# Kernel optimization log

Hardware: AMD Instinct MI355X
Metric: run time of the kernel (lower is better)

The kernel has to match this reference:

```python
import jax, jax.numpy as jnp
import numpy as np

K = 7
KK = K * K  # 49 taps
MID = (KK - 1) // 2  # 24

def _ring_ids():
    # Map each of the 49 kernel taps to its attention ring channel:
    # 0 = center, 1 = inner 3x3 ring, 2 = 5x5 ring, 3 = outer 7x7 ring.
    line7 = [j for j in range(KK) if 0 <= j <= 7 or 13 <= j <= 14 or 20 <= j <= 21 or 27 <= j <= 28 or 34 <= j <= 35 or 41 <= j <= 48]
    line5 = [j for j in range(KK) if 8 <= j <= 12 or j in (15, 19, 22, 26, 29, 33) or 36 <= j <= 40]
    line3 = [j for j in range(KK) if 16 <= j <= 18 or j in (23, 25) or 30 <= j <= 32]
    ring = np.zeros(KK, dtype=np.int32)
    ring[line7] = 3
    ring[line5] = 2
    ring[line3] = 1
    ring[MID] = 0
    return jnp.asarray(ring)

_RING = _ring_ids()


def setup_inputs() -> dict:
    key = jax.random.key(0)
    k1, k2, k3, k4 = jax.random.split(key, 4)
    bs, h, w, iters = 4, 256, 320, 6
    hw = h * w
    return {
        "kernel": jax.random.normal(k1, (bs, KK, hw), dtype=jnp.float32),
        "input": jax.random.normal(k2, (bs, 1, h, w), dtype=jnp.float32),
        "input0": jax.random.normal(k3, (bs, 1, h, w), dtype=jnp.float32),
        "attention": jax.random.uniform(k4, (bs, iters, 4, hw), dtype=jnp.float32),
        "i": 2,
    }


def reference(kernel, input, input0, attention, i):
    bs, _, h, w = input.shape
    hw = h * w
    # im2col: 7x7 patches, stride 1, pad 3 -> [bs, 49, h, w] (C=1 so tap order matches F.unfold)
    patches = jax.lax.conv_general_dilated_patches(
        input, (K, K), (1, 1), [(3, 3), (3, 3)]
    ).reshape(bs, KK, hw)
    # Ring-wise attention scaling of the affinity kernel
    att = attention[:, i]              # [bs, 4, hw]
    scale = att[:, _RING, :]           # [bs, 49, hw]
    new_kernel = kernel * scale
    # Abs-sum normalization over the 49 taps
    new_kernel = new_kernel / jnp.sum(jnp.abs(new_kernel), axis=1, keepdims=True)
    # Replace the center tap with input0 values
    patches = patches.at[:, MID, :].set(input0.reshape(bs, hw))
    # Weighted local sum
    out = jnp.sum(patches * new_kernel, axis=1)
    return out.reshape(bs, 1, h, w)
```

## Files before the change

### kernel.cpp

```cpp
#include <hip/hip_runtime.h>

#define KS   7
#define KK   49
#define MIDJ 24
#define H    256
#define W    320
#define HW   (H * W)
#define BS   4
#define ITERS 6

__global__ __launch_bounds__(256) void dyspn_kernel(
    const float* __restrict__ kern,
    const float* __restrict__ input,
    const float* __restrict__ input0,
    const float* __restrict__ att,
    const int*   __restrict__ i_ptr,
    float*       __restrict__ out)
{
    const int i_sel = *i_ptr;

    int t   = blockIdx.x * blockDim.x + threadIdx.x;
    int idx = t * 2;
    if (idx >= BS * HW) return;

    int b = idx / HW;
    int p = idx - b * HW;
    int y = p / W;
    int x = p - y * W;

    const float* attb = att + ((size_t)(b * ITERS + i_sel)) * 4 * HW + p;
    float2 a0 = *(const float2*)(attb);
    float2 a1 = *(const float2*)(attb + HW);
    float2 a2 = *(const float2*)(attb + 2 * HW);
    float2 a3 = *(const float2*)(attb + 3 * HW);
    const float ar0[4] = {a0.x, a1.x, a2.x, a3.x};
    const float ar1[4] = {a0.y, a1.y, a2.y, a3.y};

    const float* kb  = kern + (size_t)b * KK * HW + p;
    const float* inb = input + (size_t)b * HW;

    float acc0 = 0.f, acc1 = 0.f, den0 = 0.f, den1 = 0.f;

#pragma unroll
    for (int j = 0; j < KK; ++j) {
        const int dy = j / KS - 3;
        const int dx = j % KS - 3;
        const int r  = max(dy < 0 ? -dy : dy,
                           dx < 0 ? -dx : dx);

        float2 kv = *(const float2*)(kb + (size_t)j * HW);
        float v0 = kv.x * ar0[r];
        float v1 = kv.y * ar1[r];
        den0 += fabsf(v0);
        den1 += fabsf(v1);

        float p0, p1;
        if (j == MIDJ) {
            float2 z = *(const float2*)(input0 + (size_t)b * HW + p);
            p0 = z.x; p1 = z.y;
        } else {
            const int yy = y + dy;
            if (yy >= 0 && yy < H) {
                const int x0 = x + dx;
                const int x1 = x0 + 1;
                const float* row = inb + yy * W;
                p0 = (x0 >= 0 && x0 < W) ? row[x0] : 0.f;
                p1 = (x1 >= 0 && x1 < W) ? row[x1] : 0.f;
            } else {
                p0 = 0.f; p1 = 0.f;
            }
        }
        acc0 += v0 * p0;
        acc1 += v1 * p1;
    }

    float2 o;
    o.x = acc0 / den0;
    o.y = acc1 / den1;
    *(float2*)(out + (size_t)b * HW + p) = o;
}

extern "C" void kernel_launch(void* const* d_in, const int* in_sizes, int n_in,
                              void* d_out, int out_size, void* d_ws, size_t ws_size,
                              hipStream_t stream) {
    const float* kern   = (const float*)d_in[0];
    const float* input  = (const float*)d_in[1];
    const float* input0 = (const float*)d_in[2];
    const float* att    = (const float*)d_in[3];
    const int*   i_ptr  = (const int*)d_in[4];
    float* out = (float*)d_out;

    const int total_threads = BS * HW / 2;
    const int block = 256;
    const int grid  = (total_threads + block - 1) / block;

    dyspn_kernel<<<grid, block, 0, stream>>>(kern, input, input0, att, i_ptr, out);
}
```

Measured before the change: 21.54 us.

## Pre-pad input into workspace to remove bounds checks, one pixel per thread

Adds a separate kernel that writes a zero-padded copy of the input into the workspace, so the main kernel can read the 7x7 neighbourhood without bounds checks. The main kernel also moves from two pixels per thread with float2 loads to one pixel per thread with scalar loads. This is meant to cut branch and predicate overhead, at the cost of an extra kernel launch, another pass over the input, and narrower loads. A bounds-checked fallback runs when the workspace is too small.

Measured after the change: 22.43 us. +4.1%, slower.

```diff
diff --git a/kernel.cpp b/kernel.cpp
--- a/kernel.cpp
+++ b/kernel.cpp
@@ -9,7 +9,79 @@
 #define BS   4
 #define ITERS 6
 
+#define PH   (H + 6)
+#define PW   328
+#define XOFF 4
+#define PAD_ELEMS (BS * PH * PW)
+
+__global__ __launch_bounds__(256) void pad_kernel(
+    const float* __restrict__ input,
+    float*       __restrict__ pad)
+{
+    int idx = blockIdx.x * blockDim.x + threadIdx.x;
+    if (idx >= PAD_ELEMS) return;
+    int b  = idx / (PH * PW);
+    int r  = idx - b * (PH * PW);
+    int yp = r / PW;
+    int xp = r - yp * PW;
+    int y  = yp - 3;
+    int x  = xp - XOFF;
+    float v = 0.f;
+    if (y >= 0 && y < H && x >= 0 && x < W)
+        v = input[(size_t)b * HW + y * W + x];
+    pad[idx] = v;
+}
+
 __global__ __launch_bounds__(256) void dyspn_kernel(
+    const float* __restrict__ kern,
+    const float* __restrict__ pad,
+    const float* __restrict__ input0,
+    const float* __restrict__ att,
+    const int*   __restrict__ i_ptr,
+    float*       __restrict__ out)
+{
+    const int i_sel = *i_ptr;
+
+    int idx = blockIdx.x * blockDim.x + threadIdx.x;
+    if (idx >= BS * HW) return;
+
+    int b = idx / HW;
+    int p = idx - b * HW;
+    int y = p / W;
+    int x = p - y * W;
+
+    const float* attb = att + ((size_t)(b * ITERS + i_sel)) * 4 * HW + p;
+    float ar[4];
+    ar[0] = attb[0];
+    ar[1] = attb[HW];
+    ar[2] = attb[2 * HW];
+    ar[3] = attb[3 * HW];
+
+    const float* kb   = kern + (size_t)b * KK * HW + p;
+    const float* padb = pad + (size_t)b * PH * PW + (y + 3) * PW + (x + XOFF);
+    const float  mid  = input0[(size_t)b * HW + p];
+
+    float acc = 0.f, den = 0.f;
+
+#pragma unroll
+    for (int j = 0; j < KK; ++j) {
+        const int dy = j / KS - 3;
+        const int dx = j % KS - 3;
+        const int r  = max(dy < 0 ? -dy : dy,
+                           dx < 0 ? -dx : dx);
+
+        float kv = kb[(size_t)j * HW];
+        float v  = kv * ar[r];
+        den += fabsf(v);
+
+        float pv = (j == MIDJ) ? mid : padb[dy * PW + dx];
+        acc = fmaf(v, pv, acc);
+    }
+
+    out[(size_t)b * HW + p] = acc / den;
+}
+
+__global__ __launch_bounds__(256) void dyspn_kernel_checked(
     const float* __restrict__ kern,
     const float* __restrict__ input,
     const float* __restrict__ input0,
@@ -18,66 +90,37 @@
     float*       __restrict__ out)
 {
     const int i_sel = *i_ptr;
-
-    int t   = blockIdx.x * blockDim.x + threadIdx.x;
-    int idx = t * 2;
+    int idx = blockIdx.x * blockDim.x + threadIdx.x;
     if (idx >= BS * HW) return;
-
     int b = idx / HW;
     int p = idx - b * HW;
     int y = p / W;
     int x = p - y * W;
 
     const float* attb = att + ((size_t)(b * ITERS + i_sel)) * 4 * HW + p;
-    float2 a0 = *(const float2*)(attb);
-    float2 a1 = *(const float2*)(attb + HW);
-    float2 a2 = *(const float2*)(attb + 2 * HW);
-    float2 a3 = *(const float2*)(attb + 3 * HW);
-    const float ar0[4] = {a0.x, a1.x, a2.x, a3.x};
-    const float ar1[4] = {a0.y, a1.y, a2.y, a3.y};
-
+    float ar[4] = {attb[0], attb[HW], attb[2 * HW], attb[3 * HW]};
     const float* kb  = kern + (size_t)b * KK * HW + p;
     const float* inb = input + (size_t)b * HW;
+    const float  mid = input0[(size_t)b * HW + p];
 
-    float acc0 = 0.f, acc1 = 0.f, den0 = 0.f, den1 = 0.f;
-
+    float acc = 0.f, den = 0.f;
 #pragma unroll
     for (int j = 0; j < KK; ++j) {
         const int dy = j / KS - 3;
         const int dx = j % KS - 3;
-        const int r  = max(dy < 0 ? -dy : dy,
-                           dx < 0 ? -dx : dx);
-
-        float2 kv = *(const float2*)(kb + (size_t)j * HW);
-        float v0 = kv.x * ar0[r];
-        float v1 = kv.y * ar1[r];
-        den0 += fabsf(v0);
-        den1 += fabsf(v1);
-
-        float p0, p1;
+        const int r  = max(dy < 0 ? -dy : dy, dx < 0 ? -dx : dx);
+        float v = kb[(size_t)j * HW] * ar[r];
+        den += fabsf(v);
+        float pv;
         if (j == MIDJ) {
-            float2 z = *(const float2*)(input0 + (size_t)b * HW + p);
-            p0 = z.x; p1 = z.y;
+            pv = mid;
         } else {
-            const int yy = y + dy;
-            if (yy >= 0 && yy < H) {
-                const int x0 = x + dx;
-                const int x1 = x0 + 1;
-                const float* row = inb + yy * W;
-                p0 = (x0 >= 0 && x0 < W) ? row[x0] : 0.f;
-                p1 = (x1 >= 0 && x1 < W) ? row[x1] : 0.f;
-            } else {
-                p0 = 0.f; p1 = 0.f;
-            }
+            int yy = y + dy, xx = x + dx;
+            pv = (yy >= 0 && yy < H && xx >= 0 && xx < W) ? inb[yy * W + xx] : 0.f;
         }
-        acc0 += v0 * p0;
-        acc1 += v1 * p1;
+        acc = fmaf(v, pv, acc);
     }
-
-    float2 o;
-    o.x = acc0 / den0;
-    o.y = acc1 / den1;
-    *(float2*)(out + (size_t)b * HW + p) = o;
+    out[(size_t)b * HW + p] = acc / den;
 }
 
 extern "C" void kernel_launch(void* const* d_in, const int* in_sizes, int n_in,
@@ -90,9 +133,16 @@
     const int*   i_ptr  = (const int*)d_in[4];
     float* out = (float*)d_out;
 
-    const int total_threads = BS * HW / 2;
     const int block = 256;
-    const int grid  = (total_threads + block - 1) / block;
+    const int grid_main = (BS * HW + block - 1) / block;
 
-    dyspn_kernel<<<grid, block, 0, stream>>>(kern, input, input0, att, i_ptr, out);
+    const size_t pad_bytes = (size_t)PAD_ELEMS * sizeof(float);
+    if (ws_size >= pad_bytes) {
+        float* pad = (float*)d_ws;
+        const int grid_pad = (PAD_ELEMS + block - 1) / block;
+        pad_kernel<<<grid_pad, block, 0, stream>>>(input, pad);
+        dyspn_kernel<<<grid_main, block, 0, stream>>>(kern, pad, input0, att, i_ptr, out);
+    } else {
+        dyspn_kernel_checked<<<grid_main, block, 0, stream>>>(kern, input, input0, att, i_ptr, out);
+    }
 }
```

## Stream kernel taps via async global-to-LDS DMA ring and stage input tile in LDS

Applied to the files above, without the earlier changes.

Replaces the two-pixels-per-thread direct-load kernel with a one-pixel-per-thread block that prefetches the 49 kernel tap planes into an LDS ring buffer using global_load_lds. Fifteen loads are kept in flight, with explicit vmcnt waits. The input neighbourhood is staged into a padded shared tile, so the stencil reads come from LDS instead of uncoalesced, bounds-checked global loads. The aim is deeper memory-level parallelism on the bandwidth-bound tap stream. In exchange it adds LDS pressure and hand-counted waitcnt logic, which is fragile if the compiler issues other vector memory ops in between.

Measured after the change: 24.55 us. +14.0%, slower.

```diff
diff --git a/kernel.cpp b/kernel.cpp
--- a/kernel.cpp
+++ b/kernel.cpp
@@ -9,7 +9,67 @@
 #define BS   4
 #define ITERS 6
 
-__global__ __launch_bounds__(256) void dyspn_kernel(
+#define PB   256
+#define BPB  (HW / PB)
+#define DR   16
+#define NFL  15
+#define TW   328
+#define TR   8
+#define TFL  (TR * TW)
+
+typedef __attribute__((address_space(3))) unsigned       lds_u32_t;
+typedef const __attribute__((address_space(1))) unsigned glb_u32_t;
+
+template<int N> __device__ __forceinline__ void waitv();
+#define WVDEF(n) template<> __device__ __forceinline__ void waitv<n>() { \
+    asm volatile("s_waitcnt vmcnt(" #n ")" ::: "memory"); }
+WVDEF(0) WVDEF(1) WVDEF(2) WVDEF(3) WVDEF(4) WVDEF(5) WVDEF(6) WVDEF(7)
+WVDEF(8) WVDEF(9) WVDEF(10) WVDEF(11) WVDEF(12) WVDEF(13) WVDEF(14) WVDEF(15)
+
+__device__ __forceinline__ void dma4(const float* g, float* l) {
+    __builtin_amdgcn_global_load_lds((glb_u32_t*)g, (lds_u32_t*)l, 4, 0, 0);
+}
+
+struct Ctx {
+    const float* kbl;
+    float*       ringw;
+    const float* ring_rd;
+    const float* tile_rd;
+    float ar0, ar1, ar2, ar3, mid;
+};
+
+template<int J>
+struct KStep {
+    static __device__ __forceinline__ void run(const Ctx& c, float& acc, float& den) {
+        constexpr int dy = J / KS - 3;
+        constexpr int dx = J % KS - 3;
+        constexpr int ady = dy < 0 ? -dy : dy;
+        constexpr int adx = dx < 0 ? -dx : dx;
+        constexpr int r   = ady > adx ? ady : adx;
+        constexpr int slot = J % DR;
+        constexpr int KC = (J <= 34) ? (NFL - 1) : (KK - 1 - J);
+
+        waitv<KC>();
+        float kv = c.ring_rd[slot * PB];
+        float a  = (r == 0) ? c.ar0 : (r == 1) ? c.ar1 : (r == 2) ? c.ar2 : c.ar3;
+        float v  = kv * a;
+        den += fabsf(v);
+        float pv = (J == MIDJ) ? c.mid
+                               : c.tile_rd[(dy + 3) * TW + (dx + 3)];
+        acc = fmaf(v, pv, acc);
+
+        if constexpr (J + NFL < KK) {
+            constexpr int jn = J + NFL;
+            dma4(c.kbl + (size_t)jn * HW, c.ringw + (jn % DR) * PB);
+        }
+        KStep<J + 1>::run(c, acc, den);
+    }
+};
+template<> struct KStep<KK> {
+    static __device__ __forceinline__ void run(const Ctx&, float&, float&) {}
+};
+
+__global__ __launch_bounds__(PB) void dyspn_dma(
     const float* __restrict__ kern,
     const float* __restrict__ input,
     const float* __restrict__ input0,
@@ -17,67 +77,59 @@
     const int*   __restrict__ i_ptr,
     float*       __restrict__ out)
 {
+    __shared__ float ring[DR * PB];
+    __shared__ float tile[TFL];
+
+    const int tid = threadIdx.x;
+    const int bid = blockIdx.x;
+    const int b   = bid / BPB;
+    const int p0  = (bid - b * BPB) * PB;
+    const int p   = p0 + tid;
+    const int y   = p / W;
+    const int x   = p - y * W;
+    const int y0  = p0 / W;
+
     const int i_sel = *i_ptr;
 
-    int t   = blockIdx.x * blockDim.x + threadIdx.x;
-    int idx = t * 2;
-    if (idx >= BS * HW) return;
+    const float* ab = att + ((size_t)(b * ITERS + i_sel)) * 4 * HW + p;
+    float ar0 = ab[0], ar1 = ab[HW], ar2 = ab[2 * HW], ar3 = ab[3 * HW];
+    float mid = input0[(size_t)b * HW + p];
+    asm volatile("" :: "v"(ar0), "v"(ar1), "v"(ar2), "v"(ar3), "v"(mid));
 
-    int b = idx / HW;
-    int p = idx - b * HW;
-    int y = p / W;
-    int x = p - y * W;
+    #pragma unroll
+    for (int k = 0; k < (TFL + PB - 1) / PB; ++k) {
+        int idx = tid + k * PB;
+        if (idx < TFL) {
+            int rr = idx / TW;
+            int cc = idx - rr * TW;
+            int gy = y0 - 3 + rr;
+            int gx = cc - 4;
+            float v = 0.f;
+            if (gy >= 0 && gy < H && gx >= 0 && gx < W)
+                v = input[(size_t)b * HW + gy * W + gx];
+            tile[idx] = v;
+        }
+    }
+    __syncthreads();
 
-    const float* attb = att + ((size_t)(b * ITERS + i_sel)) * 4 * HW + p;
-    float2 a0 = *(const float2*)(attb);
-    float2 a1 = *(const float2*)(attb + HW);
-    float2 a2 = *(const float2*)(attb + 2 * HW);
-    float2 a3 = *(const float2*)(attb + 3 * HW);
-    const float ar0[4] = {a0.x, a1.x, a2.x, a3.x};
-    const float ar1[4] = {a0.y, a1.y, a2.y, a3.y};
+    Ctx c;
+    c.kbl     = kern + (size_t)b * KK * HW + p0 + tid;
+    c.ringw   = ring + (tid & 192);
+    c.ring_rd = ring + tid;
+    {
+        const int tb = ((y - y0) + 3) * TW + (x + 4);
+        c.tile_rd = tile + (tb - 3 * TW - 3);
+    }
+    c.ar0 = ar0; c.ar1 = ar1; c.ar2 = ar2; c.ar3 = ar3; c.mid = mid;
 
-    const float* kb  = kern + (size_t)b * KK * HW + p;
-    const float* inb = input + (size_t)b * HW;
+    #pragma unroll
+    for (int jp = 0; jp < NFL; ++jp)
+        dma4(c.kbl + (size_t)jp * HW, c.ringw + jp * PB);
 
-    float acc0 = 0.f, acc1 = 0.f, den0 = 0.f, den1 = 0.f;
+    float acc = 0.f, den = 0.f;
+    KStep<0>::run(c, acc, den);
 
-#pragma unroll
-    for (int j = 0; j < KK; ++j) {
-        const int dy = j / KS - 3;
-        const int dx = j % KS - 3;
-        const int r  = max(dy < 0 ? -dy : dy,
-                           dx < 0 ? -dx : dx);
-
-        float2 kv = *(const float2*)(kb + (size_t)j * HW);
-        float v0 = kv.x * ar0[r];
-        float v1 = kv.y * ar1[r];
-        den0 += fabsf(v0);
-        den1 += fabsf(v1);
-
-        float p0, p1;
-        if (j == MIDJ) {
-            float2 z = *(const float2*)(input0 + (size_t)b * HW + p);
-            p0 = z.x; p1 = z.y;
-        } else {
-            const int yy = y + dy;
-            if (yy >= 0 && yy < H) {
-                const int x0 = x + dx;
-                const int x1 = x0 + 1;
-                const float* row = inb + yy * W;
-                p0 = (x0 >= 0 && x0 < W) ? row[x0] : 0.f;
-                p1 = (x1 >= 0 && x1 < W) ? row[x1] : 0.f;
-            } else {
-                p0 = 0.f; p1 = 0.f;
-            }
-        }
-        acc0 += v0 * p0;
-        acc1 += v1 * p1;
-    }
-
-    float2 o;
-    o.x = acc0 / den0;
-    o.y = acc1 / den1;
-    *(float2*)(out + (size_t)b * HW + p) = o;
+    out[(size_t)b * HW + p] = acc / den;
 }
 
 extern "C" void kernel_launch(void* const* d_in, const int* in_sizes, int n_in,
@@ -90,9 +142,6 @@
     const int*   i_ptr  = (const int*)d_in[4];
     float* out = (float*)d_out;
 
-    const int total_threads = BS * HW / 2;
-    const int block = 256;
-    const int grid  = (total_threads + block - 1) / block;
-
-    dyspn_kernel<<<grid, block, 0, stream>>>(kern, input, input0, att, i_ptr, out);
+    const int grid = BS * BPB;
+    dyspn_dma<<<grid, PB, 0, stream>>>(kern, input, input0, att, i_ptr, out);
 }
```
